# Optimization experiments

Measured on AMD Instinct MI355X. Metric: run time of the kernel, lower is better.

Reference implementation:

```python
import jax, jax.numpy as jnp
import numpy as np

N_BATCH, T = 65536, 256
SURROGATE_SLOPE = 5.0


def setup_inputs() -> dict:
    key = jax.random.key(0)
    k1, k2, k3, k4 = jax.random.split(key, 4)
    x = jax.random.normal(k1, (N_BATCH, T), dtype=jnp.float32)
    beta = jax.random.normal(k2, (), dtype=jnp.float32)
    threshold = jax.random.uniform(k3, (), dtype=jnp.float32)  # kept positive like a sane threshold init
    init_rand = jax.random.uniform(k4, (N_BATCH,), dtype=jnp.float32)  # torch.rand(N_batch)
    return {"x": x, "beta": beta, "threshold": threshold, "init_rand": init_rand}


def reference(x, beta, threshold, init_rand):
    # feasible_beta = sigmoid(beta); forward uses RAW threshold (not softplus)
    fb = jax.nn.sigmoid(beta)
    # memory init: rand * threshold.detach()
    m0 = init_rand * jax.lax.stop_gradient(threshold)

    def step(m, xt):
        m_new = fb * m + xt                      # StateUpdate
        surplus = m_new - threshold
        hard = (surplus >= 0).astype(x.dtype)    # forward spike
        soft = jax.nn.sigmoid(surplus * SURROGATE_SLOPE)  # surrogate grad path
        spike = jax.lax.stop_gradient(hard) + soft - jax.lax.stop_gradient(soft)
        m_post = m_new - jax.lax.stop_gradient(spike) * threshold  # StatePostupdate
        # torch records the PRE-step memory (initial m0, then previous post-update m)
        return m_post, (spike, m)

    _, (spikes_tn, mems_tn) = jax.lax.scan(step, m0, x.T)  # scan over T
    return spikes_tn.T, mems_tn.T  # each (N_batch, T)
```

## Files before the change

### kernel.cpp

```cpp
#include <hip/hip_runtime.h>
#include <math.h>


#define N_BATCH 65536
#define T_STEPS 256
#define ROWS    64
#define CHUNK   64
#define NCHUNK  (T_STEPS / CHUNK)
#define STRIDE  (CHUNK + 1)

__global__ __launch_bounds__(64) void snn_fwd_kernel(
    const float* __restrict__ x,
    const float* __restrict__ beta_p,
    const float* __restrict__ thr_p,
    const float* __restrict__ init_rand,
    float* __restrict__ out)
{
#pragma clang fp contract(off)
    __shared__ float ss[ROWS * STRIDE];
    __shared__ float ms[ROWS * STRIDE];

    const int t   = threadIdx.x;
    const int row = blockIdx.x * ROWS + t;

    const float thr = thr_p[0];
    const float fb = (float)(1.0 / (1.0 + exp(-(double)beta_p[0])));

    float m = init_rand[row] * thr;

    const float4* __restrict__ xr =
        reinterpret_cast<const float4*>(x) + (size_t)row * (T_STEPS / 4);
    float* __restrict__ s_out = out;
    float* __restrict__ m_out = out + (size_t)N_BATCH * T_STEPS;

    for (int cc = 0; cc < NCHUNK; ++cc) {
        float* __restrict__ srow = ss + t * STRIDE;
        float* __restrict__ mrow = ms + t * STRIDE;
#pragma unroll
        for (int i = 0; i < CHUNK / 4; ++i) {
            const float4 xv = xr[cc * (CHUNK / 4) + i];
            const float xe[4] = {xv.x, xv.y, xv.z, xv.w};
#pragma unroll
            for (int j = 0; j < 4; ++j) {
                mrow[4 * i + j] = m;
                float prod = fb * m;
                float mn   = prod + xe[j];
                float su   = mn - thr;
                srow[4 * i + j] = (su >= 0.0f) ? 1.0f : 0.0f;
                m = (su >= 0.0f) ? su : mn;
            }
        }
        __syncthreads();

        const int k = t & 15;
#pragma unroll
        for (int p = 0; p < 16; ++p) {
            const int rr = (t >> 4) + 4 * p;
            const int la = rr * STRIDE + 4 * k;
            float4 sv, mv;
            sv.x = ss[la];     sv.y = ss[la + 1];
            sv.z = ss[la + 2]; sv.w = ss[la + 3];
            mv.x = ms[la];     mv.y = ms[la + 1];
            mv.z = ms[la + 2]; mv.w = ms[la + 3];
            const size_t g = (size_t)(blockIdx.x * ROWS + rr) * T_STEPS
                           + cc * CHUNK + 4 * k;
            *reinterpret_cast<float4*>(s_out + g) = sv;
            *reinterpret_cast<float4*>(m_out + g) = mv;
        }
        __syncthreads();
    }
}

extern "C" void kernel_launch(void* const* d_in, const int* in_sizes, int n_in,
                              void* d_out, int out_size, void* d_ws, size_t ws_size,
                              hipStream_t stream) {
    const float* x         = (const float*)d_in[0];
    const float* beta      = (const float*)d_in[1];
    const float* threshold = (const float*)d_in[2];
    const float* init_rand = (const float*)d_in[3];
    float* out             = (float*)d_out;

    const int threads = ROWS;
    const int blocks  = N_BATCH / ROWS;
    snn_fwd_kernel<<<blocks, threads, 0, stream>>>(x, beta, threshold, init_rand, out);
}
```

Baseline: 39.09 us.

## Prefetch next x chunk into registers, drop barriers, use nontemporal stores

```diff
diff --git a/kernel.cpp b/kernel.cpp
--- a/kernel.cpp
+++ b/kernel.cpp
@@ -7,7 +7,12 @@
 #define ROWS    64
 #define CHUNK   64
 #define NCHUNK  (T_STEPS / CHUNK)
+#define C4      (CHUNK / 4)
 #define STRIDE  (CHUNK + 1)
+
+#define LDS_FENCE() asm volatile("s_waitcnt lgkmcnt(0)" ::: "memory")
+
+typedef float f32x4 __attribute__((ext_vector_type(4)));
 
 __global__ __launch_bounds__(64) void snn_fwd_kernel(
     const float* __restrict__ x,
@@ -28,46 +33,61 @@
 
     float m = init_rand[row] * thr;
 
-    const float4* __restrict__ xr =
-        reinterpret_cast<const float4*>(x) + (size_t)row * (T_STEPS / 4);
+    const f32x4* __restrict__ xr =
+        reinterpret_cast<const f32x4*>(x) + (size_t)row * (T_STEPS / 4);
     float* __restrict__ s_out = out;
     float* __restrict__ m_out = out + (size_t)N_BATCH * T_STEPS;
 
+    f32x4 xbuf[C4];
+#pragma unroll
+    for (int i = 0; i < C4; ++i) xbuf[i] = xr[i];
+
+#pragma unroll
     for (int cc = 0; cc < NCHUNK; ++cc) {
+        f32x4 xnext[C4];
+        if (cc + 1 < NCHUNK) {
+#pragma unroll
+            for (int i = 0; i < C4; ++i) xnext[i] = xr[(cc + 1) * C4 + i];
+        }
+
         float* __restrict__ srow = ss + t * STRIDE;
         float* __restrict__ mrow = ms + t * STRIDE;
 #pragma unroll
-        for (int i = 0; i < CHUNK / 4; ++i) {
-            const float4 xv = xr[cc * (CHUNK / 4) + i];
-            const float xe[4] = {xv.x, xv.y, xv.z, xv.w};
+        for (int i = 0; i < C4; ++i) {
+            const f32x4 xv = xbuf[i];
 #pragma unroll
             for (int j = 0; j < 4; ++j) {
                 mrow[4 * i + j] = m;
                 float prod = fb * m;
-                float mn   = prod + xe[j];
+                float mn   = prod + xv[j];
                 float su   = mn - thr;
                 srow[4 * i + j] = (su >= 0.0f) ? 1.0f : 0.0f;
                 m = (su >= 0.0f) ? su : mn;
             }
         }
-        __syncthreads();
+        LDS_FENCE();
 
         const int k = t & 15;
 #pragma unroll
         for (int p = 0; p < 16; ++p) {
             const int rr = (t >> 4) + 4 * p;
             const int la = rr * STRIDE + 4 * k;
-            float4 sv, mv;
+            f32x4 sv, mv;
             sv.x = ss[la];     sv.y = ss[la + 1];
             sv.z = ss[la + 2]; sv.w = ss[la + 3];
             mv.x = ms[la];     mv.y = ms[la + 1];
             mv.z = ms[la + 2]; mv.w = ms[la + 3];
             const size_t g = (size_t)(blockIdx.x * ROWS + rr) * T_STEPS
                            + cc * CHUNK + 4 * k;
-            *reinterpret_cast<float4*>(s_out + g) = sv;
-            *reinterpret_cast<float4*>(m_out + g) = mv;
+            __builtin_nontemporal_store(sv, reinterpret_cast<f32x4*>(s_out + g));
+            __builtin_nontemporal_store(mv, reinterpret_cast<f32x4*>(m_out + g));
         }
-        __syncthreads();
+        LDS_FENCE();
+
+        if (cc + 1 < NCHUNK) {
+#pragma unroll
+            for (int i = 0; i < C4; ++i) xbuf[i] = xnext[i];
+        }
     }
 }
 
```

Result: faster. 36.18 us (-7.4%).
